# Kernel tuning notes

Measured on AMD Instinct MI355X. Metric: run time of the kernel, lower is better.

## Reference

```python
import jax, jax.numpy as jnp
import numpy as np

B, S, D = 8, 2048, 512
EPS = 1e-6
ROPE_THETA = 10000.0


def setup_inputs() -> dict:
    key = jax.random.key(0)
    ks = jax.random.split(key, 8)
    scale = 0.02
    return {
        "x": jax.random.normal(ks[0], (B, S, D), dtype=jnp.float32),
        "conv_w": jax.random.normal(ks[1], (D, D, 3), dtype=jnp.float32) * scale,
        "conv_b": jnp.zeros((D,), dtype=jnp.float32),
        "pre_g": jnp.ones((D,), dtype=jnp.float32),
        "q_g": jnp.ones((D,), dtype=jnp.float32),
        "k_g": jnp.ones((D,), dtype=jnp.float32),
        "Wq": jax.random.normal(ks[2], (D, D), dtype=jnp.float32) * scale,
        "Wk": jax.random.normal(ks[3], (D, D), dtype=jnp.float32) * scale,
        "Wv": jax.random.normal(ks[4], (D, D), dtype=jnp.float32) * scale,
    }


def _rmsnorm(x, g, eps=EPS):
    ms = jnp.mean(jnp.square(x), axis=-1, keepdims=True)
    return x * jax.lax.rsqrt(ms + eps) * g


def _rope_tables(seq_len, head_dim, dtype=jnp.float32):
    inv = 1.0 / (ROPE_THETA ** (jnp.arange(0, head_dim, 2, dtype=dtype) / head_dim))
    freqs = jnp.arange(seq_len, dtype=dtype)[:, None] * inv[None, :]  # [S, D/2]
    return jnp.cos(freqs), jnp.sin(freqs)


def _apply_rope(x, cos, sin):
    # x: [B, S, D]; treat last dim as D/2 complex pairs (interleaved real/imag)
    b, s, d = x.shape
    xr = x.reshape(b, s, d // 2, 2)
    x0, x1 = xr[..., 0], xr[..., 1]
    c = cos[None, :, :]
    sn = sin[None, :, :]
    o0 = x0 * c - x1 * sn
    o1 = x0 * sn + x1 * c
    return jnp.stack([o0, o1], axis=-1).reshape(b, s, d)


def reference(x, conv_w, conv_b, pre_g, q_g, k_g, Wq, Wk, Wv):
    b, s, d = x.shape
    # Conv1d over sequence axis (kernel 3, padding 1)
    xc = jnp.transpose(x, (0, 2, 1))  # [B, D, S]
    xc = jax.lax.conv_general_dilated(
        xc, conv_w, window_strides=(1,), padding=[(1, 1)],
        dimension_numbers=("NCH", "OIH", "NCH"))
    xc = xc + conv_b[None, :, None]
    x_norm = _rmsnorm(jnp.transpose(xc, (0, 2, 1)), pre_g)  # [B, S, D]

    q = _rmsnorm(jnp.einsum("bsd,ed->bse", x_norm, Wq), q_g)
    k = _rmsnorm(jnp.einsum("bsd,ed->bse", x_norm, Wk), k_g)
    v = jnp.einsum("bsd,ed->bse", x_norm, Wv)

    cos, sin = _rope_tables(s, d, x.dtype)
    q = _apply_rope(q, cos, sin)
    k = _apply_rope(k, cos, sin)

    scores = jnp.einsum("bqd,bkd->bqk", q, k) / jnp.sqrt(jnp.asarray(d, x.dtype))
    w = jax.nn.softmax(scores, axis=-1)  # dropout is identity in eval mode
    attended = jnp.einsum("bqk,bkd->bqd", w, v)
    out = x + attended
    return out.mean(axis=1)  # [B, D]
```

## Files before the change

### kernel.cpp

```cpp
#include <hip/hip_runtime.h>
#include <math.h>

#define BB 8
#define SS 2048
#define SSG 2050
#define DDIM 512
#define KC 1536
#define EPSV 1e-6f
#define SCALE 0.044194173824159216f

typedef unsigned short ushort_t;
using short8 = __attribute__((ext_vector_type(8))) short;
using f32x4  = __attribute__((ext_vector_type(4))) float;

__device__ inline unsigned short f2bf(float f) {
    union { float f; unsigned int u; } v; v.f = f;
    unsigned int r = v.u + 0x7FFFu + ((v.u >> 16) & 1u);
    return (unsigned short)(r >> 16);
}
__device__ inline unsigned int packbf(float a, float b) {
    return (unsigned int)f2bf(a) | ((unsigned int)f2bf(b) << 16);
}
__device__ inline float bf2f(unsigned short s) {
    union { unsigned int u; float f; } v; v.u = ((unsigned int)s) << 16; return v.f;
}

__device__ inline void gload16(const ushort_t* g, ushort_t* l) {
    __builtin_amdgcn_global_load_lds(
        (__attribute__((address_space(1))) const void*)g,
        (__attribute__((address_space(3))) void*)l, 16, 0, 0);
}

__device__ inline short8 ldswz(const ushort_t* s, int row, int c) {
    return *reinterpret_cast<const short8*>(&s[(row << 6) + ((c ^ (row & 7)) << 3)]);
}

__global__ __launch_bounds__(256) void kx_cast(const float* __restrict__ x,
                                               ushort_t* __restrict__ xbf,
                                               float* __restrict__ xsum)
{
    const int t = threadIdx.x;
    const int b = blockIdx.x;
    const int r0 = blockIdx.y * 16;
    const int c0 = 2 * t;
    if (blockIdx.y == 0) {
        *reinterpret_cast<unsigned int*>(&xbf[((size_t)b * SSG) * DDIM + c0]) = 0u;
        *reinterpret_cast<unsigned int*>(&xbf[((size_t)b * SSG + SS + 1) * DDIM + c0]) = 0u;
    }
    float s0 = 0.f, s1 = 0.f;
    for (int r = 0; r < 16; r++) {
        size_t srow = (size_t)b * SS + r0 + r;
        size_t drow = (size_t)b * SSG + 1 + r0 + r;
        float2 v = *reinterpret_cast<const float2*>(&x[srow * DDIM + c0]);
        s0 += v.x; s1 += v.y;
        *reinterpret_cast<unsigned int*>(&xbf[drow * DDIM + c0]) = packbf(v.x, v.y);
    }
    atomicAdd(&xsum[b * DDIM + c0], s0);
    atomicAdd(&xsum[b * DDIM + c0 + 1], s1);
}

__global__ __launch_bounds__(256) void k0_prep(
    const float* __restrict__ conv_w, const float* __restrict__ Wq,
    const float* __restrict__ Wk, const float* __restrict__ Wv,
    ushort_t* __restrict__ wcat, ushort_t* __restrict__ wqkv)
{
    int idx = blockIdx.x * 256 + threadIdx.x;
    {
        int o = idx / KC, kk = idx - o * KC;
        int t = kk >> 9, i = kk & 511;
        wcat[idx] = f2bf(conv_w[(size_t)o * KC + i * 3 + t]);
    }
    {
        int n = idx >> 9, d = idx & 511;
        const float* src = (n < 512) ? &Wq[(size_t)n * DDIM + d]
                         : (n < 1024) ? &Wk[(size_t)(n - 512) * DDIM + d]
                         : &Wv[(size_t)(n - 1024) * DDIM + d];
        wqkv[idx] = f2bf(*src);
    }
}

__global__ __launch_bounds__(256) void ktab(float* __restrict__ rope)
{
    const int t = threadIdx.x;
    const int r0 = blockIdx.x * 8;
    const float invf = (float)pow(10000.0, -(double)(2 * t) / (double)DDIM);
    for (int r = 0; r < 8; r++) {
        int srow = r0 + r;
        float sn, cs;
        sincosf((float)srow * invf, &sn, &cs);
        *reinterpret_cast<float2*>(&rope[((size_t)srow << 9) + 2 * t]) = make_float2(cs, sn);
    }
}

#define COMPUTE_TILE(Acur, Bcur) do { \
    _Pragma("unroll") \
    for (int half = 0; half < 2; half++) { \
        const int cb = (half << 2) | lq; \
        short8 af0 = ldswz(Acur, wm * 64 +  0 + lm, cb); \
        short8 af1 = ldswz(Acur, wm * 64 + 16 + lm, cb); \
        short8 af2 = ldswz(Acur, wm * 64 + 32 + lm, cb); \
        short8 af3 = ldswz(Acur, wm * 64 + 48 + lm, cb); \
        _Pragma("unroll") \
        for (int nt = 0; nt < 4; nt++) { \
            short8 bfv = ldswz(Bcur, wn * 64 + nt * 16 + lm, cb); \
            acc[0][nt] = __builtin_amdgcn_mfma_f32_16x16x32_bf16(af0, bfv, acc[0][nt], 0, 0, 0); \
            acc[1][nt] = __builtin_amdgcn_mfma_f32_16x16x32_bf16(af1, bfv, acc[1][nt], 0, 0, 0); \
            acc[2][nt] = __builtin_amdgcn_mfma_f32_16x16x32_bf16(af2, bfv, acc[2][nt], 0, 0, 0); \
            acc[3][nt] = __builtin_amdgcn_mfma_f32_16x16x32_bf16(af3, bfv, acc[3][nt], 0, 0, 0); \
        } \
    } } while (0)

__global__ __launch_bounds__(256) void k1b_conv(
    const ushort_t* __restrict__ xbf, const ushort_t* __restrict__ wcat,
    const float* __restrict__ conv_b, ushort_t* __restrict__ ybf, float* __restrict__ rs)
{
    __shared__ alignas(16) ushort_t As[128 * 64];
    __shared__ alignas(16) ushort_t Bs[128 * 64];
    const int t = threadIdx.x;
    const int lane = t & 63, w = t >> 6;
    const int lm = lane & 15, lq = lane >> 4;
    const int wm = w >> 1, wn = w & 1;
    const int lr = lane >> 3;
    const int lc = ((lane & 7) ^ lr) << 3;
    const int b  = blockIdx.x;
    const int s0 = blockIdx.y * 128;
    const int n0 = blockIdx.z * 128;
    const ushort_t* Ag = xbf + (size_t)b * SSG * DDIM;
    const ushort_t* Bg = wcat + (size_t)n0 * KC;

    const ushort_t* pa[4]; const ushort_t* pb[4];
    int la[4];
    #pragma unroll
    for (int i = 0; i < 4; i++) {
        const int tr = (w * 4 + i) * 8 + lr;
        pa[i] = &Ag[(size_t)(s0 + tr) * DDIM + lc];
        pb[i] = &Bg[(size_t)tr * KC + lc];
        la[i] = (w * 4 + i) * 512;
    }

    f32x4 acc[4][4];
    #pragma unroll
    for (int i = 0; i < 4; i++)
        #pragma unroll
        for (int j = 0; j < 4; j++) acc[i][j] = (f32x4){0.f, 0.f, 0.f, 0.f};

    for (int dc = 0; dc < 24; dc++) {
        __syncthreads();
        const int koff = dc * 64;
        #pragma unroll
        for (int i = 0; i < 4; i++) {
            gload16(pa[i] + koff, &As[la[i]]);
            gload16(pb[i] + koff, &Bs[la[i]]);
        }
        __syncthreads();
        COMPUTE_TILE(As, Bs);
    }

    const int rbase = s0 + wm * 64;
    const int cbase = n0 + wn * 64;
    ushort_t* yb = ybf + (size_t)b * SS * DDIM;
    float* rsb = rs + (size_t)b * SS;
    float bias[4];
    #pragma unroll
    for (int nt = 0; nt < 4; nt++) bias[nt] = conv_b[cbase + nt * 16 + lm];
    #pragma unroll
    for (int mt = 0; mt < 4; mt++) {
        float pr[4] = {0.f, 0.f, 0.f, 0.f};
        #pragma unroll
        for (int nt = 0; nt < 4; nt++) {
            #pragma unroll
            for (int r = 0; r < 4; r++) {
                float val = acc[mt][nt][r] + bias[nt];
                yb[(size_t)(rbase + mt * 16 + lq * 4 + r) * DDIM + cbase + nt * 16 + lm] = f2bf(val);
                pr[r] = fmaf(val, val, pr[r]);
            }
        }
        #pragma unroll
        for (int r = 0; r < 4; r++) {
            float p = pr[r];
            p += __shfl_xor(p, 1, 64); p += __shfl_xor(p, 2, 64);
            p += __shfl_xor(p, 4, 64); p += __shfl_xor(p, 8, 64);
            if (lm == 0) atomicAdd(&rsb[rbase + mt * 16 + lq * 4 + r], p);
        }
    }
}

__global__ __launch_bounds__(256) void k1n_norm(
    const ushort_t* __restrict__ ybf, const float* __restrict__ rs,
    const float* __restrict__ pre_g, ushort_t* __restrict__ xnbf)
{
    const int t = threadIdx.x;
    const int b = blockIdx.x;
    const int r0 = blockIdx.y * 8;
    float2 pg = *reinterpret_cast<const float2*>(&pre_g[2 * t]);
    for (int r = 0; r < 8; r++) {
        size_t row = (size_t)b * SS + r0 + r;
        float inv = rsqrtf(rs[row] * (1.0f / DDIM) + EPSV);
        unsigned int yv = *reinterpret_cast<const unsigned int*>(&ybf[row * DDIM + 2 * t]);
        float v0 = bf2f((ushort_t)(yv & 0xFFFF)), v1 = bf2f((ushort_t)(yv >> 16));
        *reinterpret_cast<unsigned int*>(&xnbf[row * DDIM + 2 * t]) =
            packbf(v0 * inv * pg.x, v1 * inv * pg.y);
    }
}

__global__ __launch_bounds__(256) void k1c_qkv(
    const ushort_t* __restrict__ xnbf, const ushort_t* __restrict__ wqkv,
    ushort_t* __restrict__ qraw, ushort_t* __restrict__ kraw, ushort_t* __restrict__ vb,
    float* __restrict__ rq, float* __restrict__ rk)
{
    __shared__ alignas(16) ushort_t As[128 * 64];
    __shared__ alignas(16) ushort_t Bs[128 * 64];
    const int t = threadIdx.x;
    const int lane = t & 63, w = t >> 6;
    const int lm = lane & 15, lq = lane >> 4;
    const int wm = w >> 1, wn = w & 1;
    const int lr = lane >> 3;
    const int lc = ((lane & 7) ^ lr) << 3;
    const int b  = blockIdx.x;
    const int s0 = blockIdx.y * 128;
    const int nt9 = blockIdx.z;
    const int n0 = nt9 * 128;
    const ushort_t* Ag = xnbf + ((size_t)b * SS + s0) * DDIM;
    const ushort_t* Bg = wqkv + (size_t)n0 * DDIM;

    const ushort_t* pa[4]; const ushort_t* pb[4];
    int la[4];
    #pragma unroll
    for (int i = 0; i < 4; i++) {
        const int tr = (w * 4 + i) * 8 + lr;
        pa[i] = &Ag[(size_t)tr * DDIM + lc];
        pb[i] = &Bg[(size_t)tr * DDIM + lc];
        la[i] = (w * 4 + i) * 512;
    }

    f32x4 acc[4][4];
    #pragma unroll
    for (int i = 0; i < 4; i++)
        #pragma unroll
        for (int j = 0; j < 4; j++) acc[i][j] = (f32x4){0.f, 0.f, 0.f, 0.f};

    for (int dc = 0; dc < 8; dc++) {
        __syncthreads();
        const int koff = dc * 64;
        #pragma unroll
        for (int i = 0; i < 4; i++) {
            gload16(pa[i] + koff, &As[la[i]]);
            gload16(pb[i] + koff, &Bs[la[i]]);
        }
        __syncthreads();
        COMPUTE_TILE(As, Bs);
    }

    const int which = nt9 >> 2;
    const int rbase = s0 + wm * 64;
    const int cbase = ((nt9 & 3) * 128) + wn * 64;
    if (which == 2) {
        ushort_t* vbb = vb + (size_t)b * SS * DDIM;
        #pragma unroll
        for (int mt = 0; mt < 4; mt++)
            #pragma unroll
            for (int nt = 0; nt < 4; nt++)
                #pragma unroll
                for (int r = 0; r < 4; r++)
                    vbb[(size_t)(rbase + mt * 16 + lq * 4 + r) * DDIM + cbase + nt * 16 + lm] =
                        f2bf(acc[mt][nt][r]);
    } else {
        ushort_t* db2 = (which ? kraw : qraw) + (size_t)b * SS * DDIM;
        float* rb = (which ? rk : rq) + (size_t)b * SS;
        #pragma unroll
        for (int mt = 0; mt < 4; mt++) {
            float pr[4] = {0.f, 0.f, 0.f, 0.f};
            #pragma unroll
            for (int nt = 0; nt < 4; nt++) {
                #pragma unroll
                for (int r = 0; r < 4; r++) {
                    float val = acc[mt][nt][r];
                    db2[(size_t)(rbase + mt * 16 + lq * 4 + r) * DDIM + cbase + nt * 16 + lm] = f2bf(val);
                    pr[r] = fmaf(val, val, pr[r]);
                }
            }
            #pragma unroll
            for (int r = 0; r < 4; r++) {
                float p = pr[r];
                p += __shfl_xor(p, 1, 64); p += __shfl_xor(p, 2, 64);
                p += __shfl_xor(p, 4, 64); p += __shfl_xor(p, 8, 64);
                if (lm == 0) atomicAdd(&rb[rbase + mt * 16 + lq * 4 + r], p);
            }
        }
    }
}

__global__ __launch_bounds__(256) void k1d_rope(
    ushort_t* q_io, ushort_t* k_io,
    const float* __restrict__ rq, const float* __restrict__ rk,
    const float* __restrict__ q_g, const float* __restrict__ k_g,
    const float* __restrict__ rope)
{
    const int t = threadIdx.x;
    const int b = blockIdx.x;
    const int r0 = blockIdx.y * 8;
    const int c0 = 2 * t;
    float qg0 = q_g[c0], qg1 = q_g[c0 + 1];
    float kg0 = k_g[c0], kg1 = k_g[c0 + 1];
    for (int r = 0; r < 8; r++) {
        int srow = r0 + r;
        size_t rowi = (size_t)b * SS + srow;
        float iq = rsqrtf(rq[rowi] * (1.0f / DDIM) + EPSV);
        float ik = rsqrtf(rk[rowi] * (1.0f / DDIM) + EPSV);
        size_t off = rowi * DDIM + c0;
        unsigned int qv = *reinterpret_cast<const unsigned int*>(&q_io[off]);
        unsigned int kv = *reinterpret_cast<const unsigned int*>(&k_io[off]);
        float q0 = bf2f((ushort_t)(qv & 0xFFFF)) * iq * qg0;
        float q1 = bf2f((ushort_t)(qv >> 16)) * iq * qg1;
        float k0v = bf2f((ushort_t)(kv & 0xFFFF)) * ik * kg0;
        float k1v = bf2f((ushort_t)(kv >> 16)) * ik * kg1;
        float2 cs2 = *reinterpret_cast<const float2*>(&rope[((size_t)srow << 9) + c0]);
        float cs = cs2.x, sn = cs2.y;
        *reinterpret_cast<unsigned int*>(&q_io[off]) = packbf(q0 * cs - q1 * sn, q0 * sn + q1 * cs);
        *reinterpret_cast<unsigned int*>(&k_io[off]) = packbf(k0v * cs - k1v * sn, k0v * sn + k1v * cs);
    }
}

__global__ __launch_bounds__(256) void k2a_rowsum(
    const ushort_t* __restrict__ qb, const ushort_t* __restrict__ kb,
    ushort_t* __restrict__ P, float* __restrict__ l)
{
    __shared__ alignas(16) ushort_t As[128 * 64];
    __shared__ alignas(16) ushort_t Bs[128 * 64];
    const int t = threadIdx.x;
    const int lane = t & 63, w = t >> 6;
    const int lm = lane & 15, lq = lane >> 4;
    const int wm = w >> 1, wn = w & 1;
    const int lr = lane >> 3;
    const int lc = ((lane & 7) ^ lr) << 3;
    const int b  = blockIdx.x;
    const int qt = blockIdx.y;
    const int kt = blockIdx.z;
    const ushort_t* Ag = qb + ((size_t)b * SS + qt * 128) * DDIM;
    const ushort_t* Bg = kb + ((size_t)b * SS + kt * 128) * DDIM;

    const ushort_t* pa[4]; const ushort_t* pb[4];
    int la[4];
    #pragma unroll
    for (int i = 0; i < 4; i++) {
        const int tr = (w * 4 + i) * 8 + lr;
        pa[i] = &Ag[(size_t)tr * DDIM + lc];
        pb[i] = &Bg[(size_t)tr * DDIM + lc];
        la[i] = (w * 4 + i) * 512;
    }

    f32x4 acc[4][4];
    #pragma unroll
    for (int i = 0; i < 4; i++)
        #pragma unroll
        for (int j = 0; j < 4; j++) acc[i][j] = (f32x4){0.f, 0.f, 0.f, 0.f};

    for (int dc = 0; dc < 8; dc++) {
        __syncthreads();
        const int koff = dc * 64;
        #pragma unroll
        for (int i = 0; i < 4; i++) {
            gload16(pa[i] + koff, &As[la[i]]);
            gload16(pb[i] + koff, &Bs[la[i]]);
        }
        __syncthreads();
        COMPUTE_TILE(As, Bs);
    }

    const int rbase = qt * 128 + wm * 64;
    const int cbase = kt * 128 + wn * 64;
    ushort_t* Pb = P + (size_t)b * SS * SS;
    float* lrow = l + (size_t)b * SS;
    #pragma unroll
    for (int mt = 0; mt < 4; mt++) {
        #pragma unroll
        for (int r = 0; r < 4; r++) {
            const int row = rbase + mt * 16 + lq * 4 + r;
            float rowp = 0.f;
            #pragma unroll
            for (int nt = 0; nt < 4; nt++) {
                float e = __expf(acc[mt][nt][r] * SCALE);
                Pb[(size_t)row * SS + cbase + nt * 16 + lm] = f2bf(e);
                rowp += e;
            }
            float p = rowp;
            p += __shfl_xor(p, 1, 64); p += __shfl_xor(p, 2, 64);
            p += __shfl_xor(p, 4, 64); p += __shfl_xor(p, 8, 64);
            if (lm == 0) atomicAdd(&lrow[row], p);
        }
    }
}

__global__ __launch_bounds__(256) void k2c_colred(
    const ushort_t* __restrict__ P, const float* __restrict__ l,
    float* __restrict__ cw)
{
    const int t = threadIdx.x;
    const int b = blockIdx.x;
    const int q0 = blockIdx.y * 128;
    const int k0 = blockIdx.z * 1024 + t * 4;
    const ushort_t* Pb = P + ((size_t)b * SS + q0) * SS;
    const float* lb = l + (size_t)b * SS + q0;
    float a0 = 0.f, a1 = 0.f, a2 = 0.f, a3 = 0.f;
    for (int q = 0; q < 128; q++) {
        float rl = 1.0f / lb[q];
        uint2 pp = *reinterpret_cast<const uint2*>(&Pb[(size_t)q * SS + k0]);
        a0 = fmaf(bf2f((ushort_t)(pp.x & 0xFFFF)), rl, a0);
        a1 = fmaf(bf2f((ushort_t)(pp.x >> 16)), rl, a1);
        a2 = fmaf(bf2f((ushort_t)(pp.y & 0xFFFF)), rl, a2);
        a3 = fmaf(bf2f((ushort_t)(pp.y >> 16)), rl, a3);
    }
    atomicAdd(&cw[(size_t)b * SS + k0], a0);
    atomicAdd(&cw[(size_t)b * SS + k0 + 1], a1);
    atomicAdd(&cw[(size_t)b * SS + k0 + 2], a2);
    atomicAdd(&cw[(size_t)b * SS + k0 + 3], a3);
}

__global__ __launch_bounds__(256) void k4_out(
    const float* __restrict__ xsum, const ushort_t* __restrict__ v,
    const float* __restrict__ cwv, float* __restrict__ out)
{
    const int b = blockIdx.x, c = blockIdx.y;
    const int t = threadIdx.x;
    const int srow0 = c * (SS / 16);
    const ushort_t* vb = v + ((size_t)b * SS + srow0) * DDIM;
    const float* cwb   = cwv + (size_t)b * SS + srow0;
    float a0 = (c == 0) ? xsum[b * DDIM + t]       : 0.f;
    float a1 = (c == 0) ? xsum[b * DDIM + t + 256] : 0.f;
    for (int r = 0; r < SS / 16; r++) {
        float w = cwb[r];
        a0 += w * bf2f(vb[(size_t)r * DDIM + t]);
        a1 += w * bf2f(vb[(size_t)r * DDIM + t + 256]);
    }
    atomicAdd(&out[b * DDIM + t],       a0 * (1.0f / SS));
    atomicAdd(&out[b * DDIM + t + 256], a1 * (1.0f / SS));
}

extern "C" void kernel_launch(void* const* d_in, const int* in_sizes, int n_in,
                              void* d_out, int out_size, void* d_ws, size_t ws_size,
                              hipStream_t stream)
{
    const float* x      = (const float*)d_in[0];
    const float* conv_w = (const float*)d_in[1];
    const float* conv_b = (const float*)d_in[2];
    const float* pre_g  = (const float*)d_in[3];
    const float* q_g    = (const float*)d_in[4];
    const float* k_g    = (const float*)d_in[5];
    const float* Wq     = (const float*)d_in[6];
    const float* Wk     = (const float*)d_in[7];
    const float* Wv     = (const float*)d_in[8];
    float* out          = (float*)d_out;

    const size_t NTOK  = (size_t)BB * SS * DDIM;
    const size_t NTOKG = (size_t)BB * SSG * DDIM;
    char* p = (char*)d_ws;
    ushort_t* xbf = (ushort_t*)p; p += NTOKG * 2;
    ushort_t* ybf = (ushort_t*)p; p += NTOK * 2;
    ushort_t* xn  = (ushort_t*)p; p += NTOK * 2;
    char* padreg = p;             p += NTOK * 2;
    ushort_t* qio = (ushort_t*)p; p += NTOK * 2;
    ushort_t* kio = (ushort_t*)p; p += NTOK * 2;
    ushort_t* vb  = (ushort_t*)p; p += NTOK * 2;
    ushort_t* wcat = (ushort_t*)p; p += (size_t)DDIM * KC * 2;
    ushort_t* wqkv = (ushort_t*)p; p += (size_t)KC * DDIM * 2;
    float* rs   = (float*)p; p += (size_t)BB * SS * 4;
    float* rq   = (float*)p; p += (size_t)BB * SS * 4;
    float* rk   = (float*)p; p += (size_t)BB * SS * 4;
    float* lbuf = (float*)p; p += (size_t)BB * SS * 4;
    float* cwb  = (float*)p; p += (size_t)BB * SS * 4;
    float* xsum = (float*)p; p += (size_t)BB * DDIM * 4;

    ushort_t* Pbuf = xbf;
    float* rope = (float*)padreg;

    (void)hipMemsetAsync(d_out, 0, (size_t)out_size * sizeof(float), stream);
    (void)hipMemsetAsync(rs, 0, ((size_t)BB * SS * 5 + (size_t)BB * DDIM) * sizeof(float), stream);

    kx_cast<<<dim3(BB, SS / 16), 256, 0, stream>>>(x, xbf, xsum);
    k0_prep<<<dim3(DDIM * KC / 256), 256, 0, stream>>>(conv_w, Wq, Wk, Wv, wcat, wqkv);
    ktab<<<dim3(SS / 8), 256, 0, stream>>>(rope);
    k1b_conv<<<dim3(BB, SS / 128, 4), 256, 0, stream>>>(xbf, wcat, conv_b, ybf, rs);
    k1n_norm<<<dim3(BB, SS / 8), 256, 0, stream>>>(ybf, rs, pre_g, xn);
    k1c_qkv<<<dim3(BB, SS / 128, 12), 256, 0, stream>>>(xn, wqkv, qio, kio, vb, rq, rk);
    k1d_rope<<<dim3(BB, SS / 8), 256, 0, stream>>>(qio, kio, rq, rk, q_g, k_g, rope);
    k2a_rowsum<<<dim3(BB, SS / 128, SS / 128), 256, 0, stream>>>(qio, kio, Pbuf, lbuf);
    k2c_colred<<<dim3(BB, SS / 128, SS / 1024), 256, 0, stream>>>(Pbuf, lbuf, cwb);
    k4_out<<<dim3(BB, 16), 256, 0, stream>>>(xsum, vb, cwb, out);
}
```

Baseline: 275.6 us.

## Fold pre-RMSNorm into QKV GEMM epilogue and merge rope table into prep

The pre-norm gain is folded into the bf16 QKV weights during prep, and the per-row RMS scale is applied in the QKV GEMM epilogue, so the GEMM reads the raw conv output directly. This removes the separate normalization kernel and its full read-write pass over the activations. The rope table generation is also merged into the weight prep kernel, saving one launch. Normalization now happens after bf16 rounding of unnormalized values, which changes rounding slightly.

After: 271.0 us. Within noise of the previous version (-1.7%).

```diff
diff --git a/kernel.cpp b/kernel.cpp
--- a/kernel.cpp
+++ b/kernel.cpp
@@ -62,7 +62,9 @@
 __global__ __launch_bounds__(256) void k0_prep(
     const float* __restrict__ conv_w, const float* __restrict__ Wq,
     const float* __restrict__ Wk, const float* __restrict__ Wv,
-    ushort_t* __restrict__ wcat, ushort_t* __restrict__ wqkv)
+    const float* __restrict__ pre_g,
+    ushort_t* __restrict__ wcat, ushort_t* __restrict__ wqkv,
+    float* __restrict__ rope)
 {
     int idx = blockIdx.x * 256 + threadIdx.x;
     {
@@ -75,20 +77,18 @@
         const float* src = (n < 512) ? &Wq[(size_t)n * DDIM + d]
                          : (n < 1024) ? &Wk[(size_t)(n - 512) * DDIM + d]
                          : &Wv[(size_t)(n - 1024) * DDIM + d];
-        wqkv[idx] = f2bf(*src);
-    }
-}
-
-__global__ __launch_bounds__(256) void ktab(float* __restrict__ rope)
-{
-    const int t = threadIdx.x;
-    const int r0 = blockIdx.x * 8;
-    const float invf = (float)pow(10000.0, -(double)(2 * t) / (double)DDIM);
-    for (int r = 0; r < 8; r++) {
-        int srow = r0 + r;
-        float sn, cs;
-        sincosf((float)srow * invf, &sn, &cs);
-        *reinterpret_cast<float2*>(&rope[((size_t)srow << 9) + 2 * t]) = make_float2(cs, sn);
+        wqkv[idx] = f2bf(*src * pre_g[d]);
+    }
+    if (blockIdx.x < SS / 8) {
+        const int t = threadIdx.x;
+        const int r0 = blockIdx.x * 8;
+        const float invf = (float)pow(10000.0, -(double)(2 * t) / (double)DDIM);
+        for (int r = 0; r < 8; r++) {
+            int srow = r0 + r;
+            float sn, cs;
+            sincosf((float)srow * invf, &sn, &cs);
+            *reinterpret_cast<float2*>(&rope[((size_t)srow << 9) + 2 * t]) = make_float2(cs, sn);
+        }
     }
 }
 
@@ -185,26 +185,9 @@
     }
 }
 
-__global__ __launch_bounds__(256) void k1n_norm(
+__global__ __launch_bounds__(256) void k1c_qkv(
     const ushort_t* __restrict__ ybf, const float* __restrict__ rs,
-    const float* __restrict__ pre_g, ushort_t* __restrict__ xnbf)
-{
-    const int t = threadIdx.x;
-    const int b = blockIdx.x;
-    const int r0 = blockIdx.y * 8;
-    float2 pg = *reinterpret_cast<const float2*>(&pre_g[2 * t]);
-    for (int r = 0; r < 8; r++) {
-        size_t row = (size_t)b * SS + r0 + r;
-        float inv = rsqrtf(rs[row] * (1.0f / DDIM) + EPSV);
-        unsigned int yv = *reinterpret_cast<const unsigned int*>(&ybf[row * DDIM + 2 * t]);
-        float v0 = bf2f((ushort_t)(yv & 0xFFFF)), v1 = bf2f((ushort_t)(yv >> 16));
-        *reinterpret_cast<unsigned int*>(&xnbf[row * DDIM + 2 * t]) =
-            packbf(v0 * inv * pg.x, v1 * inv * pg.y);
-    }
-}
-
-__global__ __launch_bounds__(256) void k1c_qkv(
-    const ushort_t* __restrict__ xnbf, const ushort_t* __restrict__ wqkv,
+    const ushort_t* __restrict__ wqkv,
     ushort_t* __restrict__ qraw, ushort_t* __restrict__ kraw, ushort_t* __restrict__ vb,
     float* __restrict__ rq, float* __restrict__ rk)
 {
@@ -220,7 +203,7 @@
     const int s0 = blockIdx.y * 128;
     const int nt9 = blockIdx.z;
     const int n0 = nt9 * 128;
-    const ushort_t* Ag = xnbf + ((size_t)b * SS + s0) * DDIM;
+    const ushort_t* Ag = ybf + ((size_t)b * SS + s0) * DDIM;
     const ushort_t* Bg = wqkv + (size_t)n0 * DDIM;
 
     const ushort_t* pa[4]; const ushort_t* pb[4];
@@ -254,6 +237,14 @@
     const int which = nt9 >> 2;
     const int rbase = s0 + wm * 64;
     const int cbase = ((nt9 & 3) * 128) + wn * 64;
+    const float* rsb = rs + (size_t)b * SS;
+    float inv[4][4];
+    #pragma unroll
+    for (int mt = 0; mt < 4; mt++)
+        #pragma unroll
+        for (int r = 0; r < 4; r++)
+            inv[mt][r] = rsqrtf(rsb[rbase + mt * 16 + lq * 4 + r] * (1.0f / DDIM) + EPSV);
+
     if (which == 2) {
         ushort_t* vbb = vb + (size_t)b * SS * DDIM;
         #pragma unroll
@@ -263,7 +254,7 @@
                 #pragma unroll
                 for (int r = 0; r < 4; r++)
                     vbb[(size_t)(rbase + mt * 16 + lq * 4 + r) * DDIM + cbase + nt * 16 + lm] =
-                        f2bf(acc[mt][nt][r]);
+                        f2bf(acc[mt][nt][r] * inv[mt][r]);
     } else {
         ushort_t* db2 = (which ? kraw : qraw) + (size_t)b * SS * DDIM;
         float* rb = (which ? rk : rq) + (size_t)b * SS;
@@ -274,7 +265,7 @@
             for (int nt = 0; nt < 4; nt++) {
                 #pragma unroll
                 for (int r = 0; r < 4; r++) {
-                    float val = acc[mt][nt][r];
+                    float val = acc[mt][nt][r] * inv[mt][r];
                     db2[(size_t)(rbase + mt * 16 + lq * 4 + r) * DDIM + cbase + nt * 16 + lm] = f2bf(val);
                     pr[r] = fmaf(val, val, pr[r]);
                 }
@@ -456,7 +447,7 @@
     char* p = (char*)d_ws;
     ushort_t* xbf = (ushort_t*)p; p += NTOKG * 2;
     ushort_t* ybf = (ushort_t*)p; p += NTOK * 2;
-    ushort_t* xn  = (ushort_t*)p; p += NTOK * 2;
+     p += NTOK * 2;
     char* padreg = p;             p += NTOK * 2;
     ushort_t* qio = (ushort_t*)p; p += NTOK * 2;
     ushort_t* kio = (ushort_t*)p; p += NTOK * 2;
@@ -477,11 +468,9 @@
     (void)hipMemsetAsync(rs, 0, ((size_t)BB * SS * 5 + (size_t)BB * DDIM) * sizeof(float), stream);
 
     kx_cast<<<dim3(BB, SS / 16), 256, 0, stream>>>(x, xbf, xsum);
-    k0_prep<<<dim3(DDIM * KC / 256), 256, 0, stream>>>(conv_w, Wq, Wk, Wv, wcat, wqkv);
-    ktab<<<dim3(SS / 8), 256, 0, stream>>>(rope);
+    k0_prep<<<dim3(DDIM * KC / 256), 256, 0, stream>>>(conv_w, Wq, Wk, Wv, pre_g, wcat, wqkv, rope);
     k1b_conv<<<dim3(BB, SS / 128, 4), 256, 0, stream>>>(xbf, wcat, conv_b, ybf, rs);
-    k1n_norm<<<dim3(BB, SS / 8), 256, 0, stream>>>(ybf, rs, pre_g, xn);
-    k1c_qkv<<<dim3(BB, SS / 128, 12), 256, 0, stream>>>(xn, wqkv, qio, kio, vb, rq, rk);
+    k1c_qkv<<<dim3(BB, SS / 128, 12), 256, 0, stream>>>(ybf, rs, wqkv, qio, kio, vb, rq, rk);
     k1d_rope<<<dim3(BB, SS / 8), 256, 0, stream>>>(qio, kio, rq, rk, q_g, k_g, rope);
     k2a_rowsum<<<dim3(BB, SS / 128, SS / 128), 256, 0, stream>>>(qio, kio, Pbuf, lbuf);
     k2c_colred<<<dim3(BB, SS / 128, SS / 1024), 256, 0, stream>>>(Pbuf, lbuf, cwb);
```
